# Optimization experiments

Hardware: AMD Instinct MI355X
Metric: run time of the kernel (lower is better)

## Reference

```python
import jax, jax.numpy as jnp
import numpy as np

N = 96            # num_orbitals
C = 128           # hidden_channels
H = 16            # num_heads
D = C // H        # head_dim = 8
LN_EPS = 1e-6


def setup_inputs() -> dict:
    key = jax.random.key(0)
    ks = jax.random.split(key, 10)
    x = jax.random.normal(ks[0], (N, C), dtype=jnp.float32)
    H_core = jax.random.normal(ks[1], (N, N), dtype=jnp.float32)
    X = jax.random.normal(ks[2], (N, N), dtype=jnp.float32)
    eri = jax.random.normal(ks[3], (N, N, N, N), dtype=jnp.float32)
    P_init = jax.random.normal(ks[4], (N, N), dtype=jnp.float32)
    # learned params (flax Dense: kernel [in, out]; LayerNorm scale/bias)
    ln_scale = jnp.ones((C,), dtype=jnp.float32)
    ln_bias = jnp.zeros((C,), dtype=jnp.float32)
    Wqkv = jax.random.normal(ks[5], (C, 3 * C), dtype=jnp.float32) / np.sqrt(C)
    Wout = jax.random.normal(ks[6], (C, C), dtype=jnp.float32) / np.sqrt(C)
    bout = jnp.zeros((C,), dtype=jnp.float32)
    return {"x": x, "H_core": H_core, "X": X, "eri": eri, "P_init": P_init,
            "ln_scale": ln_scale, "ln_bias": ln_bias,
            "Wqkv": Wqkv, "Wout": Wout, "bout": bout}


def reference(x, H_core, X, eri, P_init, ln_scale, ln_bias, Wqkv, Wout, bout):
    # quantum bias terms
    J = jnp.einsum('kl,ijkl->ij', P_init, eri)      # Coulomb
    K = jnp.einsum('ij,ikjl->kl', P_init, eri)      # exchange
    diff_JK = J - K / 2
    L = X @ H_core @ X.T
    # LayerNorm over feature dim
    mu = jnp.mean(x, axis=-1, keepdims=True)
    var = jnp.mean((x - mu) ** 2, axis=-1, keepdims=True)
    xn = (x - mu) * jax.lax.rsqrt(var + LN_EPS) * ln_scale + ln_bias
    # QKV projection (no bias)
    qkv = xn @ Wqkv                                   # [N, 3C]
    q, k, v = jnp.split(qkv, 3, axis=-1)
    q = q.reshape(N, H, D); k = k.reshape(N, H, D); v = v.reshape(N, H, D)
    qk = jnp.einsum('ihd,jhd->hij', q, k) / jnp.sqrt(jnp.float32(D))  # [H,N,N]
    # per-head-slice bias injection
    qk = qk.at[0:2].add(H_core[None])
    qk = qk.at[2:4].add(diff_JK[None])
    qk = qk.at[4:6].add(L[None])
    attn = jax.nn.softmax(qk, axis=-1)
    out = jnp.einsum('hij,jhd->ihd', attn, v).reshape(N, C)
    return out @ Wout + bout
```

## Files before the change

### kernel.cpp

```cpp
#include <hip/hip_runtime.h>

#define NORB 96
#define NN 9216

typedef float f32x4 __attribute__((ext_vector_type(4)));

__global__ __launch_bounds__(192) void prep_kernel(
    const float* __restrict__ X, const float* __restrict__ Hc,
    const float* __restrict__ x, const float* __restrict__ ln_s,
    const float* __restrict__ ln_b, const float* __restrict__ Wqkv,
    float* __restrict__ Lm, float* __restrict__ Km, float* __restrict__ qkv) {
  const int blk = blockIdx.x;
  const int t = threadIdx.x;
  if (blk < 96) {
    const int i = blk;
    __shared__ float Xs[NN];
    __shared__ float tmp[NORB];
    for (int f = t; f < NN; f += 192) Xs[f] = X[f];
    if (t < NORB) Km[i * NORB + t] = 0.f;
    __syncthreads();
    if (t < NORB) {
      float acc = 0.f;
      for (int m = 0; m < NORB; ++m) acc += Xs[i * NORB + m] * Hc[m * NORB + t];
      tmp[t] = acc;
    }
    __syncthreads();
    if (t < NORB) {
      float acc = 0.f;
      for (int k = 0; k < NORB; ++k) acc += tmp[k] * Xs[t * NORB + k];
      Lm[i * NORB + t] = acc;
    }
  } else {
    const int i = blk - 96;
    __shared__ float xn[128];
    __shared__ float red[3];
    float v = (t < 128) ? x[i * 128 + t] : 0.f;
    float s = v;
#pragma unroll
    for (int off = 32; off; off >>= 1) s += __shfl_down(s, off);
    if ((t & 63) == 0) red[t >> 6] = s;
    __syncthreads();
    const float mu = (red[0] + red[1] + red[2]) * (1.f / 128.f);
    __syncthreads();
    const float dv = (t < 128) ? (v - mu) : 0.f;
    s = dv * dv;
#pragma unroll
    for (int off = 32; off; off >>= 1) s += __shfl_down(s, off);
    if ((t & 63) == 0) red[t >> 6] = s;
    __syncthreads();
    const float var = (red[0] + red[1] + red[2]) * (1.f / 128.f);
    if (t < 128) xn[t] = dv * rsqrtf(var + 1e-6f) * ln_s[t] + ln_b[t];
    __syncthreads();
#pragma unroll
    for (int jj = 0; jj < 2; ++jj) {
      const int j = t + jj * 192;
      float acc = 0.f;
      for (int c = 0; c < 128; ++c) acc += xn[c] * Wqkv[c * 384 + j];
      qkv[i * 384 + j] = acc;
    }
  }
}

__global__ __launch_bounds__(384) void jk_kernel(
    const float* __restrict__ eri, const float* __restrict__ P,
    float* __restrict__ Jm, float* __restrict__ Km) {
  const int blk = blockIdx.x;
  const int b = blk % NORB;
  const int ap = blk / NORB;
  const int a0 = 2 * ap, a1 = a0 + 1;
  const int t = threadIdx.x;
  const int x = t % 24;
  const int y = t / 24;
  const f32x4* __restrict__ slab0 =
      (const f32x4*)(eri + (size_t)(a0 * NORB + b) * NN);
  const f32x4* __restrict__ slab1 =
      (const f32x4*)(eri + (size_t)(a1 * NORB + b) * NN);
  const f32x4* __restrict__ P4 = (const f32x4*)P;

  __shared__ float pa_sh[2][NORB];
  __shared__ float klp[16][NORB];
  __shared__ float js[2][6];

  if (t < NORB) pa_sh[0][t] = P[a0 * NORB + t];
  else if (t < 2 * NORB) pa_sh[1][t - NORB] = P[a1 * NORB + (t - NORB)];

  f32x4 pvr[6];
#pragma unroll
  for (int k = 0; k < 6; ++k) pvr[k] = P4[t + 384 * k];
  __syncthreads();

  float jp0 = 0.f, jp1 = 0.f;
  f32x4 kacc = {0.f, 0.f, 0.f, 0.f};
#pragma unroll
  for (int k = 0; k < 6; ++k) {
    const f32x4 v0 = __builtin_nontemporal_load(&slab0[t + 384 * k]);
    const f32x4 v1 = __builtin_nontemporal_load(&slab1[t + 384 * k]);
    const float pa0 = pa_sh[0][y + 16 * k];
    const float pa1 = pa_sh[1][y + 16 * k];
    jp0 += v0.x * pvr[k].x + v0.y * pvr[k].y + v0.z * pvr[k].z + v0.w * pvr[k].w;
    jp1 += v1.x * pvr[k].x + v1.y * pvr[k].y + v1.z * pvr[k].z + v1.w * pvr[k].w;
    kacc += pa0 * v0 + pa1 * v1;
  }

  klp[y][4 * x + 0] = kacc.x;
  klp[y][4 * x + 1] = kacc.y;
  klp[y][4 * x + 2] = kacc.z;
  klp[y][4 * x + 3] = kacc.w;
#pragma unroll
  for (int off = 32; off; off >>= 1) {
    jp0 += __shfl_down(jp0, off);
    jp1 += __shfl_down(jp1, off);
  }
  if ((t & 63) == 0) {
    js[0][t >> 6] = jp0;
    js[1][t >> 6] = jp1;
  }
  __syncthreads();
  if (t < 2) {
    const float* j6 = js[t];
    Jm[(a0 + t) * NORB + b] = j6[0] + j6[1] + j6[2] + j6[3] + j6[4] + j6[5];
  }
  if (t < NORB) {
    float kk = 0.f;
#pragma unroll
    for (int yy = 0; yy < 16; ++yy) kk += klp[yy][t];
    atomicAdd(&Km[b * NORB + t], kk);
  }
}

__global__ __launch_bounds__(256) void attn_proj_kernel(
    const float* __restrict__ qkv, const float* __restrict__ Hc,
    const float* __restrict__ Jm, const float* __restrict__ Km,
    const float* __restrict__ Lm, const float* __restrict__ Wout,
    const float* __restrict__ bout, float* __restrict__ y) {
  const int i = blockIdx.x;
  const int t = threadIdx.x;
  __shared__ float qs[128];
  __shared__ float ps[16][97];
  __shared__ float aout_sh[128];

  if (t < 128) qs[t] = qkv[i * 384 + t];
  __syncthreads();

  const int h = t >> 4;
  const int jg = t & 15;
  float sc[6];
#pragma unroll
  for (int m = 0; m < 6; ++m) {
    const int j = jg + 16 * m;
    const float* kr = qkv + j * 384 + 128 + h * 8;
    float d = 0.f;
#pragma unroll
    for (int dd = 0; dd < 8; ++dd) d += qs[h * 8 + dd] * kr[dd];
    d *= 0.3535533905932738f;
    const int ij = i * NORB + j;
    if (h < 2) d += Hc[ij];
    else if (h < 4) d += Jm[ij] - 0.5f * Km[ij];
    else if (h < 6) d += Lm[ij];
    sc[m] = d;
  }
  float mx = sc[0];
#pragma unroll
  for (int m = 1; m < 6; ++m) mx = fmaxf(mx, sc[m]);
#pragma unroll
  for (int off = 8; off; off >>= 1) mx = fmaxf(mx, __shfl_xor(mx, off, 16));
  float sm = 0.f;
#pragma unroll
  for (int m = 0; m < 6; ++m) {
    sc[m] = __expf(sc[m] - mx);
    sm += sc[m];
  }
#pragma unroll
  for (int off = 8; off; off >>= 1) sm += __shfl_xor(sm, off, 16);
  const float inv = 1.f / sm;
#pragma unroll
  for (int m = 0; m < 6; ++m) ps[h][jg + 16 * m] = sc[m] * inv;
  __syncthreads();

  if (t < 128) {
    const int h2 = t >> 3;
    float acc = 0.f;
#pragma unroll 8
    for (int j = 0; j < NORB; ++j) acc += ps[h2][j] * qkv[j * 384 + 256 + t];
    aout_sh[t] = acc;
  }
  __syncthreads();
  if (t < 128) {
    float acc = bout[t];
#pragma unroll 8
    for (int c = 0; c < 128; ++c) acc += aout_sh[c] * Wout[c * 128 + t];
    y[i * 128 + t] = acc;
  }
}

extern "C" void kernel_launch(void* const* d_in, const int* in_sizes, int n_in,
                              void* d_out, int out_size, void* d_ws,
                              size_t ws_size, hipStream_t stream) {
  const float* x    = (const float*)d_in[0];
  const float* Hc   = (const float*)d_in[1];
  const float* X    = (const float*)d_in[2];
  const float* eri  = (const float*)d_in[3];
  const float* P    = (const float*)d_in[4];
  const float* ln_s = (const float*)d_in[5];
  const float* ln_b = (const float*)d_in[6];
  const float* Wqkv = (const float*)d_in[7];
  const float* Wout = (const float*)d_in[8];
  const float* bout = (const float*)d_in[9];
  float* y = (float*)d_out;

  float* ws  = (float*)d_ws;
  float* Jm  = ws;
  float* Km  = ws + NN;
  float* Lm  = ws + 2 * NN;
  float* qkv = ws + 3 * NN;

  prep_kernel<<<192, 192, 0, stream>>>(X, Hc, x, ln_s, ln_b, Wqkv, Lm, Km, qkv);

  jk_kernel<<<4608, 384, 0, stream>>>(eri, P, Jm, Km);

  attn_proj_kernel<<<NORB, 256, 0, stream>>>(qkv, Hc, Jm, Km, Lm, Wout, bout, y);
}
```

Measured before the change: 75.12 us.

## Fuse prep and J/K kernels; replace K atomics with per-slab partials

Merges the prep (L, LayerNorm, QKV) work and the ERI J/K contraction into one launch, with one block per (a,b) slab instead of two slabs per block. The atomicAdd accumulation of K is replaced by writing 96 partial K matrices to workspace, which the attention kernel reduces per row. This removes a kernel launch, the Km zero-init ordering dependency and the atomic contention. In exchange it adds about 3.5 MB of partial writes and reads, and it halves the per-block work on the eri stream.

```diff
diff --git a/kernel.cpp b/kernel.cpp
--- a/kernel.cpp
+++ b/kernel.cpp
@@ -5,141 +5,129 @@
 
 typedef float f32x4 __attribute__((ext_vector_type(4)));
 
-__global__ __launch_bounds__(192) void prep_kernel(
+__global__ __launch_bounds__(384) void mega_kernel(
+    const float* __restrict__ eri, const float* __restrict__ P,
     const float* __restrict__ X, const float* __restrict__ Hc,
     const float* __restrict__ x, const float* __restrict__ ln_s,
     const float* __restrict__ ln_b, const float* __restrict__ Wqkv,
-    float* __restrict__ Lm, float* __restrict__ Km, float* __restrict__ qkv) {
+    float* __restrict__ Jm, float* __restrict__ Kpart,
+    float* __restrict__ Lm, float* __restrict__ qkv) {
   const int blk = blockIdx.x;
   const int t = threadIdx.x;
+
   if (blk < 96) {
     const int i = blk;
-    __shared__ float Xs[NN];
+    __shared__ float xrow[NORB];
     __shared__ float tmp[NORB];
-    for (int f = t; f < NN; f += 192) Xs[f] = X[f];
-    if (t < NORB) Km[i * NORB + t] = 0.f;
+    if (t < NORB) xrow[t] = X[i * NORB + t];
     __syncthreads();
     if (t < NORB) {
       float acc = 0.f;
-      for (int m = 0; m < NORB; ++m) acc += Xs[i * NORB + m] * Hc[m * NORB + t];
+      for (int m = 0; m < NORB; ++m) acc += xrow[m] * Hc[m * NORB + t];
       tmp[t] = acc;
     }
     __syncthreads();
     if (t < NORB) {
       float acc = 0.f;
-      for (int k = 0; k < NORB; ++k) acc += tmp[k] * Xs[t * NORB + k];
+      for (int k = 0; k < NORB; ++k) acc += tmp[k] * X[t * NORB + k];
       Lm[i * NORB + t] = acc;
     }
-  } else {
+    return;
+  }
+  if (blk < 192) {
     const int i = blk - 96;
     __shared__ float xn[128];
-    __shared__ float red[3];
+    __shared__ float red[2];
     float v = (t < 128) ? x[i * 128 + t] : 0.f;
     float s = v;
 #pragma unroll
     for (int off = 32; off; off >>= 1) s += __shfl_down(s, off);
-    if ((t & 63) == 0) red[t >> 6] = s;
-    __syncthreads();
-    const float mu = (red[0] + red[1] + red[2]) * (1.f / 128.f);
+    if (t == 0 || t == 64) red[t >> 6] = s;
+    __syncthreads();
+    const float mu = (red[0] + red[1]) * (1.f / 128.f);
     __syncthreads();
     const float dv = (t < 128) ? (v - mu) : 0.f;
     s = dv * dv;
 #pragma unroll
     for (int off = 32; off; off >>= 1) s += __shfl_down(s, off);
-    if ((t & 63) == 0) red[t >> 6] = s;
-    __syncthreads();
-    const float var = (red[0] + red[1] + red[2]) * (1.f / 128.f);
+    if (t == 0 || t == 64) red[t >> 6] = s;
+    __syncthreads();
+    const float var = (red[0] + red[1]) * (1.f / 128.f);
     if (t < 128) xn[t] = dv * rsqrtf(var + 1e-6f) * ln_s[t] + ln_b[t];
     __syncthreads();
-#pragma unroll
-    for (int jj = 0; jj < 2; ++jj) {
-      const int j = t + jj * 192;
-      float acc = 0.f;
-      for (int c = 0; c < 128; ++c) acc += xn[c] * Wqkv[c * 384 + j];
-      qkv[i * 384 + j] = acc;
-    }
-  }
-}
-
-__global__ __launch_bounds__(384) void jk_kernel(
-    const float* __restrict__ eri, const float* __restrict__ P,
-    float* __restrict__ Jm, float* __restrict__ Km) {
-  const int blk = blockIdx.x;
-  const int b = blk % NORB;
-  const int ap = blk / NORB;
-  const int a0 = 2 * ap, a1 = a0 + 1;
-  const int t = threadIdx.x;
-  const int x = t % 24;
+    float acc = 0.f;
+    for (int c = 0; c < 128; ++c) acc += xn[c] * Wqkv[c * 384 + t];
+    qkv[i * 384 + t] = acc;
+    return;
+  }
+
+  const int ab = blk - 192;
+  const int a = ab / NORB;
+  const int b = ab - a * NORB;
+  const int x24 = t % 24;
   const int y = t / 24;
-  const f32x4* __restrict__ slab0 =
-      (const f32x4*)(eri + (size_t)(a0 * NORB + b) * NN);
-  const f32x4* __restrict__ slab1 =
-      (const f32x4*)(eri + (size_t)(a1 * NORB + b) * NN);
+  const f32x4* __restrict__ slab4 = (const f32x4*)(eri + (size_t)ab * NN);
   const f32x4* __restrict__ P4 = (const f32x4*)P;
 
-  __shared__ float pa_sh[2][NORB];
+  __shared__ float pa_sh[NORB];
   __shared__ float klp[16][NORB];
-  __shared__ float js[2][6];
-
-  if (t < NORB) pa_sh[0][t] = P[a0 * NORB + t];
-  else if (t < 2 * NORB) pa_sh[1][t - NORB] = P[a1 * NORB + (t - NORB)];
+  __shared__ float js[6];
+
+  if (t < NORB) pa_sh[t] = P[a * NORB + t];
 
   f32x4 pvr[6];
 #pragma unroll
   for (int k = 0; k < 6; ++k) pvr[k] = P4[t + 384 * k];
   __syncthreads();
 
-  float jp0 = 0.f, jp1 = 0.f;
-  f32x4 kacc = {0.f, 0.f, 0.f, 0.f};
+  float jp = 0.f, k0 = 0.f, k1 = 0.f, k2 = 0.f, k3 = 0.f;
 #pragma unroll
   for (int k = 0; k < 6; ++k) {
-    const f32x4 v0 = __builtin_nontemporal_load(&slab0[t + 384 * k]);
-    const f32x4 v1 = __builtin_nontemporal_load(&slab1[t + 384 * k]);
-    const float pa0 = pa_sh[0][y + 16 * k];
-    const float pa1 = pa_sh[1][y + 16 * k];
-    jp0 += v0.x * pvr[k].x + v0.y * pvr[k].y + v0.z * pvr[k].z + v0.w * pvr[k].w;
-    jp1 += v1.x * pvr[k].x + v1.y * pvr[k].y + v1.z * pvr[k].z + v1.w * pvr[k].w;
-    kacc += pa0 * v0 + pa1 * v1;
-  }
-
-  klp[y][4 * x + 0] = kacc.x;
-  klp[y][4 * x + 1] = kacc.y;
-  klp[y][4 * x + 2] = kacc.z;
-  klp[y][4 * x + 3] = kacc.w;
-#pragma unroll
-  for (int off = 32; off; off >>= 1) {
-    jp0 += __shfl_down(jp0, off);
-    jp1 += __shfl_down(jp1, off);
-  }
-  if ((t & 63) == 0) {
-    js[0][t >> 6] = jp0;
-    js[1][t >> 6] = jp1;
-  }
-  __syncthreads();
-  if (t < 2) {
-    const float* j6 = js[t];
-    Jm[(a0 + t) * NORB + b] = j6[0] + j6[1] + j6[2] + j6[3] + j6[4] + j6[5];
-  }
+    const f32x4 v = __builtin_nontemporal_load(&slab4[t + 384 * k]);
+    const float pa = pa_sh[y + 16 * k];
+    jp += v.x * pvr[k].x + v.y * pvr[k].y + v.z * pvr[k].z + v.w * pvr[k].w;
+    k0 += pa * v.x;
+    k1 += pa * v.y;
+    k2 += pa * v.z;
+    k3 += pa * v.w;
+  }
+
+  klp[y][4 * x24 + 0] = k0;
+  klp[y][4 * x24 + 1] = k1;
+  klp[y][4 * x24 + 2] = k2;
+  klp[y][4 * x24 + 3] = k3;
+#pragma unroll
+  for (int off = 32; off; off >>= 1) jp += __shfl_down(jp, off);
+  if ((t & 63) == 0) js[t >> 6] = jp;
+  __syncthreads();
+  if (t == 0) Jm[ab] = js[0] + js[1] + js[2] + js[3] + js[4] + js[5];
   if (t < NORB) {
     float kk = 0.f;
 #pragma unroll
     for (int yy = 0; yy < 16; ++yy) kk += klp[yy][t];
-    atomicAdd(&Km[b * NORB + t], kk);
+    Kpart[(size_t)a * NN + b * NORB + t] = kk;
   }
 }
 
 __global__ __launch_bounds__(256) void attn_proj_kernel(
     const float* __restrict__ qkv, const float* __restrict__ Hc,
-    const float* __restrict__ Jm, const float* __restrict__ Km,
+    const float* __restrict__ Jm, const float* __restrict__ Kpart,
     const float* __restrict__ Lm, const float* __restrict__ Wout,
     const float* __restrict__ bout, float* __restrict__ y) {
   const int i = blockIdx.x;
   const int t = threadIdx.x;
   __shared__ float qs[128];
+  __shared__ float kmrow[NORB];
   __shared__ float ps[16][97];
   __shared__ float aout_sh[128];
 
   if (t < 128) qs[t] = qkv[i * 384 + t];
+  if (t < NORB) {
+    float kk = 0.f;
+#pragma unroll 8
+    for (int a = 0; a < NORB; ++a) kk += Kpart[(size_t)a * NN + i * NORB + t];
+    kmrow[t] = kk;
+  }
   __syncthreads();
 
   const int h = t >> 4;
@@ -155,7 +143,7 @@
     d *= 0.3535533905932738f;
     const int ij = i * NORB + j;
     if (h < 2) d += Hc[ij];
-    else if (h < 4) d += Jm[ij] - 0.5f * Km[ij];
+    else if (h < 4) d += Jm[ij] - 0.5f * kmrow[j];
     else if (h < 6) d += Lm[ij];
     sc[m] = d;
   }
@@ -208,15 +196,15 @@
   const float* bout = (const float*)d_in[9];
   float* y = (float*)d_out;
 
-  float* ws  = (float*)d_ws;
-  float* Jm  = ws;
-  float* Km  = ws + NN;
-  float* Lm  = ws + 2 * NN;
-  float* qkv = ws + 3 * NN;
-
-  prep_kernel<<<192, 192, 0, stream>>>(X, Hc, x, ln_s, ln_b, Wqkv, Lm, Km, qkv);
-
-  jk_kernel<<<4608, 384, 0, stream>>>(eri, P, Jm, Km);
-
-  attn_proj_kernel<<<NORB, 256, 0, stream>>>(qkv, Hc, Jm, Km, Lm, Wout, bout, y);
+  float* ws    = (float*)d_ws;
+  float* Jm    = ws;
+  float* Lm    = ws + NN;
+  float* qkv   = ws + 2 * NN;
+  float* Kpart = ws + 2 * NN + 36864;
+
+  mega_kernel<<<192 + NN, 384, 0, stream>>>(eri, P, X, Hc, x, ln_s, ln_b,
+                                            Wqkv, Jm, Kpart, Lm, qkv);
+
+  attn_proj_kernel<<<NORB, 256, 0, stream>>>(qkv, Hc, Jm, Kpart, Lm, Wout,
+                                             bout, y);
 }
```

New measurement: 73.31 us. 1.02x faster.
